# Kernel optimization log

Measured on AMD Instinct MI355X. Metric: run time of the kernel, lower is better.

The kernel has to match this reference:

```python
import jax, jax.numpy as jnp
import numpy as np

S = 8192      # s: number of persons/nodes
F = 1024      # feature_len
A = 256       # attn_len
SIGMA_X, SIGMA_Y = 4.0, 1.0
EPS_VALID = 1e-8
EPS_DIS = 1e-4


def setup_inputs() -> dict:
    key = jax.random.key(0)
    ks = jax.random.split(key, 8)
    batch_data = jax.random.normal(ks[0], (S, F), dtype=jnp.float32)
    xywh = jax.random.uniform(ks[1], (S, 4), dtype=jnp.float32)  # positive -> all rows valid
    actor_weights = jax.random.uniform(ks[2], (S,), dtype=jnp.float32)
    avg_pos = jax.random.uniform(ks[3], (S, 2), dtype=jnp.float32)
    # learned params (kaiming-ish init, zero bias as in original)
    W_h = jax.random.normal(ks[4], (F, 2), dtype=jnp.float32) * (2.0 / F) ** 0.5
    b_h = jnp.zeros((2,), dtype=jnp.float32)
    W_g = jax.random.normal(ks[5], (F, A), dtype=jnp.float32) * (2.0 / F) ** 0.5
    b_g = jnp.zeros((A,), dtype=jnp.float32)
    return {
        "batch_data": batch_data, "xywh": xywh, "OW": 1920, "OH": 1080,
        "actor_weights": actor_weights, "avg_pos": avg_pos,
        "W_h": W_h, "b_h": b_h, "W_g": W_g, "b_g": b_g, "num_person": S,
    }


def reference(batch_data, xywh, OW, OH, actor_weights, avg_pos, W_h, b_h, W_g, b_g, num_person):
    # highlight_fc + tanh -> predicted offsets [S,2]
    hp = jnp.tanh(batch_data @ W_h + b_h)
    hx = hp[:, 0] * xywh[:, 2] * SIGMA_X + xywh[:, 0]  # [S]
    hy = hp[:, 1] * xywh[:, 3] * SIGMA_Y + xywh[:, 1]  # [S]

    # gcn_fc + relu -> node messages [S,A]
    targets = jax.nn.relu(batch_data @ W_g + b_g)

    # valid rows/cols: torch loop skips i/j with sum(xywh) < 1e-8
    valid = jnp.sum(xywh, axis=1) >= EPS_VALID  # [S] bool

    # pairwise inverse-distance weights [S,S] (the memory-bound core)
    dx = hx[:, None] - xywh[None, :, 0]
    dy = hy[:, None] - xywh[None, :, 1]
    dis = jnp.sqrt(dx * dx + dy * dy)
    pair_valid = valid[:, None] & valid[None, :]
    w = jnp.where(pair_valid, 1.0 / (dis + EPS_DIS), 0.0)
    row_sum = jnp.sum(w, axis=1, keepdims=True)
    w = jnp.where(valid[:, None], w / jnp.maximum(row_sum, 1e-30), 0.0)

    targets_weighted = w @ targets  # [S,A]
    return (targets_weighted, hp)
```

## Files before the change

### kernel.cpp

```cpp
#include <hip/hip_runtime.h>
#include <math.h>
#include <stdint.h>

typedef __attribute__((ext_vector_type(8))) short short8;
typedef __attribute__((ext_vector_type(4))) float f32x4;

__device__ __forceinline__ uint32_t cvt_pk_bf16(float lo, float hi) {
  uint32_t r;
  asm("v_cvt_pk_bf16_f32 %0, %1, %2" : "=v"(r) : "v"(lo), "v"(hi));
  return r;
}

__device__ __forceinline__ float wfun(float hx, float hy, float cx, float cy) {
  float dx = hx - cx, dy = hy - cy;
  float d = __builtin_amdgcn_sqrtf(fmaf(dx, dx, dy * dy));
  return __builtin_amdgcn_rcpf(d + 1e-4f);
}

__global__ __launch_bounds__(256) void k_head(
    const float* __restrict__ batch, const float* __restrict__ xywh,
    const float* __restrict__ W_h, const float* __restrict__ b_h,
    float* __restrict__ hp_out, float* __restrict__ hx, float* __restrict__ hy,
    float* __restrict__ validf, float2* __restrict__ cxy, int S, int F) {
  int wid = threadIdx.x >> 6;
  int lane = threadIdx.x & 63;
  int row = blockIdx.x * 4 + wid;
  if (row >= S) return;
  const float4* brow = (const float4*)(batch + (size_t)row * F);
  const float4* wh4 = (const float4*)W_h;
  int nf4 = F >> 2;
  float acc0 = 0.f, acc1 = 0.f;
  for (int k4 = lane; k4 < nf4; k4 += 64) {
    float4 b = brow[k4];
    float4 wa = wh4[2 * k4];
    float4 wb = wh4[2 * k4 + 1];
    acc0 += b.x * wa.x + b.y * wa.z + b.z * wb.x + b.w * wb.z;
    acc1 += b.x * wa.y + b.y * wa.w + b.z * wb.y + b.w * wb.w;
  }
  #pragma unroll
  for (int off = 32; off; off >>= 1) {
    acc0 += __shfl_xor(acc0, off, 64);
    acc1 += __shfl_xor(acc1, off, 64);
  }
  if (lane == 0) {
    float hp0 = tanhf(acc0 + b_h[0]);
    float hp1 = tanhf(acc1 + b_h[1]);
    float4 xy = ((const float4*)xywh)[row];
    hp_out[2 * row] = hp0;
    hp_out[2 * row + 1] = hp1;
    hx[row] = hp0 * xy.z * 4.0f + xy.x;
    hy[row] = hp1 * xy.w * 1.0f + xy.y;
    bool v = (xy.x + xy.y + xy.z + xy.w >= 1e-8f);
    validf[row] = v ? 1.0f : 0.0f;
    cxy[row] = v ? make_float2(xy.x, xy.y) : make_float2(1e30f, 1e30f);
  }
}

__global__ __launch_bounds__(256) void k_prep_w(
    const float* __restrict__ Wg, uint16_t* __restrict__ WgT, int F, int A) {
  int idx = blockIdx.x * 256 + threadIdx.x;
  int a = idx % A;
  int k0 = (idx / A) * 8;
  if (k0 >= F) return;
  float f[8];
  #pragma unroll
  for (int e = 0; e < 8; ++e) f[e] = Wg[(size_t)(k0 + e) * A + a];
  uint4 v;
  v.x = cvt_pk_bf16(f[0], f[1]);
  v.y = cvt_pk_bf16(f[2], f[3]);
  v.z = cvt_pk_bf16(f[4], f[5]);
  v.w = cvt_pk_bf16(f[6], f[7]);
  *(uint4*)(WgT + (size_t)a * F + k0) = v;
}

__global__ __launch_bounds__(256) void k_targets_mfma(
    const float* __restrict__ batch, const uint16_t* __restrict__ WgT,
    const float* __restrict__ bg, uint16_t* __restrict__ tgt2,
    int S, int F, int A) {
  int t = threadIdx.x;
  int lane = t & 63, wid = t >> 6;
  int wm = wid >> 1, wn = wid & 1;
  int i0 = blockIdx.y * 32;
  int row = i0 + wm * 16 + (lane & 15);
  int kch = lane >> 4;
  const float* ab = batch + (size_t)row * F + kch * 8;
  int ncol0 = blockIdx.x * 128 + wn * 64 + (lane & 15);
  const uint16_t* bb = WgT + (size_t)ncol0 * F + kch * 8;

  f32x4 acc[4] = {};
  float4 a0 = *(const float4*)(ab);
  float4 a1 = *(const float4*)(ab + 4);
  short8 bf[4];
  #pragma unroll
  for (int nf = 0; nf < 4; ++nf)
    bf[nf] = *(const short8*)(bb + (size_t)nf * 16 * F);

  for (int k0 = 0; k0 < F; k0 += 32) {
    int kn = (k0 + 32 < F) ? k0 + 32 : 0;
    float4 na0 = *(const float4*)(ab + kn);
    float4 na1 = *(const float4*)(ab + kn + 4);
    short8 nbf[4];
    #pragma unroll
    for (int nf = 0; nf < 4; ++nf)
      nbf[nf] = *(const short8*)(bb + kn + (size_t)nf * 16 * F);
    union { short8 s; uint32_t u[4]; } af;
    af.u[0] = cvt_pk_bf16(a0.x, a0.y);
    af.u[1] = cvt_pk_bf16(a0.z, a0.w);
    af.u[2] = cvt_pk_bf16(a1.x, a1.y);
    af.u[3] = cvt_pk_bf16(a1.z, a1.w);
    #pragma unroll
    for (int nf = 0; nf < 4; ++nf)
      acc[nf] = __builtin_amdgcn_mfma_f32_16x16x32_bf16(af.s, bf[nf], acc[nf], 0, 0, 0);
    a0 = na0; a1 = na1;
    #pragma unroll
    for (int nf = 0; nf < 4; ++nf) bf[nf] = nbf[nf];
  }

  int jb = blockIdx.y;
  int rloc = wm * 16 + (lane >> 4) * 4;
  #pragma unroll
  for (int nf = 0; nf < 4; ++nf) {
    int col = ncol0 + nf * 16;
    float b = bg[col];
    float o0 = fmaxf(acc[nf][0] + b, 0.f);
    float o1 = fmaxf(acc[nf][1] + b, 0.f);
    float o2 = fmaxf(acc[nf][2] + b, 0.f);
    float o3 = fmaxf(acc[nf][3] + b, 0.f);
    uint2 pk;
    pk.x = cvt_pk_bf16(o0, o1);
    pk.y = cvt_pk_bf16(o2, o3);
    *(uint2*)(tgt2 + ((size_t)jb * A + col) * 32 + rloc) = pk;
  }
}

__global__ __launch_bounds__(1024, 4) void k_gather_v17(
    const uint16_t* __restrict__ tgt2, const float2* __restrict__ cxy,
    const float* __restrict__ hx, const float* __restrict__ hy,
    const float* __restrict__ validf, float* __restrict__ out, int S, int A) {
  __shared__ uint16_t Bt[4][256][40];
  __shared__ uint32_t Af[4][2][64][4];
  __shared__ float comb[32][260];
  __shared__ float rs_l[4][32][8];
  __shared__ float scale_s[32];

  int t = threadIdx.x;
  int lane = t & 63, wid = t >> 6;
  int kg = wid >> 2;
  int wn = wid & 3;
  int i0 = blockIdx.x * 32;
  int kch = lane >> 4;
  int n0 = wn * 64 + (lane & 15);
  int NT = S / (4 * 32);
  const size_t TSTRIDE = (size_t)A * 32;

  int wkg = t >> 8;
  int v = t & 255;
  int wr = v & 31;
  int wjp8 = v >> 5;
  float hx_w = hx[i0 + wr], hy_w = hy[i0 + wr];
  int rgw = wr >> 4;
  int L0 = (wr & 15) | ((wjp8 >> 2) << 4);
  int L1 = (wr & 15) | (((wjp8 >> 2) + 2) << 4);
  int sl = wjp8 & 3;
  const float2* gCp = cxy + (size_t)wkg * (S >> 2) + 2 * wjp8;

  int scol = v;
  const uint16_t* gB0 = tgt2 + (size_t)(wkg * NT) * TSTRIDE + (size_t)scol * 32;

  f32x4 acc0[4] = {};
  f32x4 acc1[4] = {};
  float rs = 0.f;

  {
    uint4 q0 = *(const uint4*)(gB0);
    uint4 q1 = *(const uint4*)(gB0 + 8);
    uint4 q2 = *(const uint4*)(gB0 + 16);
    uint4 q3 = *(const uint4*)(gB0 + 24);
    *(uint4*)&Bt[wkg][scol][0]  = q0;
    *(uint4*)&Bt[wkg][scol][8]  = q1;
    *(uint4*)&Bt[wkg][scol][16] = q2;
    *(uint4*)&Bt[wkg][scol][24] = q3;
    float4 ca = *(const float4*)(gCp);
    float4 cb = *(const float4*)(gCp + 16);
    float wA = wfun(hx_w, hy_w, ca.x, ca.y);
    float wB = wfun(hx_w, hy_w, ca.z, ca.w);
    float wC = wfun(hx_w, hy_w, cb.x, cb.y);
    float wD = wfun(hx_w, hy_w, cb.z, cb.w);
    rs += (wA + wB) + (wC + wD);
    Af[wkg][rgw][L0][sl] = cvt_pk_bf16(wA, wB);
    Af[wkg][rgw][L1][sl] = cvt_pk_bf16(wC, wD);
  }
  __syncthreads();
  float4 ccur0 = *(const float4*)(gCp + 32);
  float4 ccur1 = *(const float4*)(gCp + 48);

  for (int ts = 0; ts < NT; ++ts) {
    int tn = (ts + 1 < NT) ? ts + 1 : 0;
    int tf = (ts + 2 < NT) ? ts + 2 : 0;

    const uint16_t* bp = gB0 + (size_t)tn * TSTRIDE;
    uint4 q0 = *(const uint4*)(bp);
    uint4 q1 = *(const uint4*)(bp + 8);
    uint4 q2 = *(const uint4*)(bp + 16);
    uint4 q3 = *(const uint4*)(bp + 24);
    float4 cf0 = *(const float4*)(gCp + (size_t)tf * 32);
    float4 cf1 = *(const float4*)(gCp + (size_t)tf * 32 + 16);

    short8 a0 = *(const short8*)&Af[kg][0][lane][0];
    short8 a1 = *(const short8*)&Af[kg][1][lane][0];
    const uint16_t* br = &Bt[kg][n0][kch * 8];
    short8 b0 = *(const short8*)(br);
    short8 b1 = *(const short8*)(br + 16 * 40);
    short8 b2 = *(const short8*)(br + 32 * 40);
    short8 b3 = *(const short8*)(br + 48 * 40);

    acc0[0] = __builtin_amdgcn_mfma_f32_16x16x32_bf16(a0, b0, acc0[0], 0, 0, 0);
    acc0[1] = __builtin_amdgcn_mfma_f32_16x16x32_bf16(a0, b1, acc0[1], 0, 0, 0);
    acc0[2] = __builtin_amdgcn_mfma_f32_16x16x32_bf16(a0, b2, acc0[2], 0, 0, 0);
    acc0[3] = __builtin_amdgcn_mfma_f32_16x16x32_bf16(a0, b3, acc0[3], 0, 0, 0);
    acc1[0] = __builtin_amdgcn_mfma_f32_16x16x32_bf16(a1, b0, acc1[0], 0, 0, 0);
    acc1[1] = __builtin_amdgcn_mfma_f32_16x16x32_bf16(a1, b1, acc1[1], 0, 0, 0);
    acc1[2] = __builtin_amdgcn_mfma_f32_16x16x32_bf16(a1, b2, acc1[2], 0, 0, 0);
    acc1[3] = __builtin_amdgcn_mfma_f32_16x16x32_bf16(a1, b3, acc1[3], 0, 0, 0);

    float wA = wfun(hx_w, hy_w, ccur0.x, ccur0.y);
    float wB = wfun(hx_w, hy_w, ccur0.z, ccur0.w);
    float wC = wfun(hx_w, hy_w, ccur1.x, ccur1.y);
    float wD = wfun(hx_w, hy_w, ccur1.z, ccur1.w);
    float g = (ts + 1 < NT) ? 1.f : 0.f;
    rs = fmaf(g, (wA + wB) + (wC + wD), rs);
    uint32_t pkA = cvt_pk_bf16(wA, wB);
    uint32_t pkB = cvt_pk_bf16(wC, wD);

    __syncthreads();

    *(uint4*)&Bt[wkg][scol][0]  = q0;
    *(uint4*)&Bt[wkg][scol][8]  = q1;
    *(uint4*)&Bt[wkg][scol][16] = q2;
    *(uint4*)&Bt[wkg][scol][24] = q3;
    Af[wkg][rgw][L0][sl] = pkA;
    Af[wkg][rgw][L1][sl] = pkB;

    __syncthreads();
    ccur0 = cf0;
    ccur1 = cf1;
  }

  rs_l[wkg][wr][wjp8] = rs;
  __syncthreads();
  if (t < 32) {
    float r = 0.f;
    #pragma unroll
    for (int k = 0; k < 4; ++k)
      #pragma unroll
      for (int jp = 0; jp < 8; ++jp) r += rs_l[k][t][jp];
    float fv = validf[i0 + t];
    scale_s[t] = (fv > 0.f) ? 1.0f / fmaxf(r, 1e-30f) : 0.f;
  }
  __syncthreads();

  int rbase = (lane >> 4) * 4;
  #pragma unroll
  for (int round = 1; round < 4; ++round) {
    if (kg == round) {
      #pragma unroll
      for (int r = 0; r < 4; ++r) {
        comb[rbase + r][n0]      = acc0[0][r];
        comb[rbase + r][n0 + 16] = acc0[1][r];
        comb[rbase + r][n0 + 32] = acc0[2][r];
        comb[rbase + r][n0 + 48] = acc0[3][r];
        comb[16 + rbase + r][n0]      = acc1[0][r];
        comb[16 + rbase + r][n0 + 16] = acc1[1][r];
        comb[16 + rbase + r][n0 + 32] = acc1[2][r];
        comb[16 + rbase + r][n0 + 48] = acc1[3][r];
      }
    }
    __syncthreads();
    if (kg == 0) {
      #pragma unroll
      for (int r = 0; r < 4; ++r) {
        acc0[0][r] += comb[rbase + r][n0];
        acc0[1][r] += comb[rbase + r][n0 + 16];
        acc0[2][r] += comb[rbase + r][n0 + 32];
        acc0[3][r] += comb[rbase + r][n0 + 48];
        acc1[0][r] += comb[16 + rbase + r][n0];
        acc1[1][r] += comb[16 + rbase + r][n0 + 16];
        acc1[2][r] += comb[16 + rbase + r][n0 + 32];
        acc1[3][r] += comb[16 + rbase + r][n0 + 48];
      }
    }
    __syncthreads();
  }

  if (kg == 0) {
    #pragma unroll
    for (int r = 0; r < 4; ++r) {
      int row0 = rbase + r;
      float s0 = scale_s[row0];
      size_t base0 = (size_t)(i0 + row0) * A;
      out[base0 + n0]      = acc0[0][r] * s0;
      out[base0 + n0 + 16] = acc0[1][r] * s0;
      out[base0 + n0 + 32] = acc0[2][r] * s0;
      out[base0 + n0 + 48] = acc0[3][r] * s0;
      int row1 = 16 + rbase + r;
      float s1 = scale_s[row1];
      size_t base1 = (size_t)(i0 + row1) * A;
      out[base1 + n0]      = acc1[0][r] * s1;
      out[base1 + n0 + 16] = acc1[1][r] * s1;
      out[base1 + n0 + 32] = acc1[2][r] * s1;
      out[base1 + n0 + 48] = acc1[3][r] * s1;
    }
  }
}

extern "C" void kernel_launch(void* const* d_in, const int* in_sizes, int n_in,
                              void* d_out, int out_size, void* d_ws, size_t ws_size,
                              hipStream_t stream) {
  const float* batch = (const float*)d_in[0];
  const float* xywh  = (const float*)d_in[1];
  const float* W_h   = (const float*)d_in[6];
  const float* b_h   = (const float*)d_in[7];
  const float* W_g   = (const float*)d_in[8];
  const float* b_g   = (const float*)d_in[9];
  int S = in_sizes[4];
  int F = in_sizes[0] / S;
  int A = in_sizes[9];

  float* out    = (float*)d_out;
  float* out_tw = out;
  float* out_hp = out + (size_t)S * A;

  uint16_t* tgt2 = (uint16_t*)d_ws;
  uint16_t* WgT  = tgt2 + (size_t)A * S;
  float* hxv = (float*)(WgT + (size_t)A * F);
  float* hyv = hxv + S;
  float* vfv = hyv + S;
  float2* cxyv = (float2*)(vfv + S);

  k_head<<<dim3((S + 3) / 4), 256, 0, stream>>>(batch, xywh, W_h, b_h,
                                                out_hp, hxv, hyv, vfv, cxyv, S, F);
  k_prep_w<<<dim3((A * F / 8 + 255) / 256), 256, 0, stream>>>(W_g, WgT, F, A);
  k_targets_mfma<<<dim3(A / 128, S / 32), 256, 0, stream>>>(batch, WgT, b_g,
                                                            tgt2, S, F, A);
  k_gather_v17<<<dim3(S / 32), 1024, 0, stream>>>(tgt2, cxyv, hxv, hyv, vfv,
                                                  out_tw, S, A);
}
```

Before: 155.9 us.

## Double-buffer gather LDS with two k-groups and widen targets GEMM tile

The gather kernel drops from four k-split wave groups (1024 threads) to two (512 threads). It double-buffers the Bt/Af shared tiles so only one barrier per iteration is needed, and replaces the three-round cross-group reduction with a single combine step. The targets GEMM now has each block compute all 256 output columns (8 MFMA tiles per wave), so each A row is loaded and converted once instead of twice. The cost is less k-parallelism per block, longer serial loops, and higher register pressure in the GEMM.

```diff
diff --git a/kernel.cpp b/kernel.cpp
--- a/kernel.cpp
+++ b/kernel.cpp
@@ -80,28 +80,28 @@
   int t = threadIdx.x;
   int lane = t & 63, wid = t >> 6;
   int wm = wid >> 1, wn = wid & 1;
-  int i0 = blockIdx.y * 32;
+  int i0 = blockIdx.x * 32;
   int row = i0 + wm * 16 + (lane & 15);
   int kch = lane >> 4;
   const float* ab = batch + (size_t)row * F + kch * 8;
-  int ncol0 = blockIdx.x * 128 + wn * 64 + (lane & 15);
+  int ncol0 = wn * 128 + (lane & 15);
   const uint16_t* bb = WgT + (size_t)ncol0 * F + kch * 8;
 
-  f32x4 acc[4] = {};
+  f32x4 acc[8] = {};
   float4 a0 = *(const float4*)(ab);
   float4 a1 = *(const float4*)(ab + 4);
-  short8 bf[4];
+  short8 bf[8];
   #pragma unroll
-  for (int nf = 0; nf < 4; ++nf)
+  for (int nf = 0; nf < 8; ++nf)
     bf[nf] = *(const short8*)(bb + (size_t)nf * 16 * F);
 
   for (int k0 = 0; k0 < F; k0 += 32) {
     int kn = (k0 + 32 < F) ? k0 + 32 : 0;
     float4 na0 = *(const float4*)(ab + kn);
     float4 na1 = *(const float4*)(ab + kn + 4);
-    short8 nbf[4];
-    #pragma unroll
-    for (int nf = 0; nf < 4; ++nf)
+    short8 nbf[8];
+    #pragma unroll
+    for (int nf = 0; nf < 8; ++nf)
       nbf[nf] = *(const short8*)(bb + kn + (size_t)nf * 16 * F);
     union { short8 s; uint32_t u[4]; } af;
     af.u[0] = cvt_pk_bf16(a0.x, a0.y);
@@ -109,17 +109,17 @@
     af.u[2] = cvt_pk_bf16(a1.x, a1.y);
     af.u[3] = cvt_pk_bf16(a1.z, a1.w);
     #pragma unroll
-    for (int nf = 0; nf < 4; ++nf)
+    for (int nf = 0; nf < 8; ++nf)
       acc[nf] = __builtin_amdgcn_mfma_f32_16x16x32_bf16(af.s, bf[nf], acc[nf], 0, 0, 0);
     a0 = na0; a1 = na1;
     #pragma unroll
-    for (int nf = 0; nf < 4; ++nf) bf[nf] = nbf[nf];
-  }
-
-  int jb = blockIdx.y;
+    for (int nf = 0; nf < 8; ++nf) bf[nf] = nbf[nf];
+  }
+
+  int jb = blockIdx.x;
   int rloc = wm * 16 + (lane >> 4) * 4;
   #pragma unroll
-  for (int nf = 0; nf < 4; ++nf) {
+  for (int nf = 0; nf < 8; ++nf) {
     int col = ncol0 + nf * 16;
     float b = bg[col];
     float o0 = fmaxf(acc[nf][0] + b, 0.f);
@@ -133,14 +133,14 @@
   }
 }
 
-__global__ __launch_bounds__(1024, 4) void k_gather_v17(
+__global__ __launch_bounds__(512, 2) void k_gather_v19(
     const uint16_t* __restrict__ tgt2, const float2* __restrict__ cxy,
     const float* __restrict__ hx, const float* __restrict__ hy,
     const float* __restrict__ validf, float* __restrict__ out, int S, int A) {
-  __shared__ uint16_t Bt[4][256][40];
-  __shared__ uint32_t Af[4][2][64][4];
+  __shared__ uint16_t Bt[2][2][256][40];
+  __shared__ uint32_t Af[2][2][2][64][4];
   __shared__ float comb[32][260];
-  __shared__ float rs_l[4][32][8];
+  __shared__ float rs_l[2][32][8];
   __shared__ float scale_s[32];
 
   int t = threadIdx.x;
@@ -150,8 +150,9 @@
   int i0 = blockIdx.x * 32;
   int kch = lane >> 4;
   int n0 = wn * 64 + (lane & 15);
-  int NT = S / (4 * 32);
+  int NT = (S >> 1) / 32;
   const size_t TSTRIDE = (size_t)A * 32;
+  const int COLS = 40;
 
   int wkg = t >> 8;
   int v = t & 255;
@@ -162,7 +163,11 @@
   int L0 = (wr & 15) | ((wjp8 >> 2) << 4);
   int L1 = (wr & 15) | (((wjp8 >> 2) + 2) << 4);
   int sl = wjp8 & 3;
-  const float2* gCp = cxy + (size_t)wkg * (S >> 2) + 2 * wjp8;
+  uint32_t* af00 = &Af[0][wkg][rgw][L0][sl];
+  uint32_t* af01 = &Af[0][wkg][rgw][L1][sl];
+  uint32_t* af10 = &Af[1][wkg][rgw][L0][sl];
+  uint32_t* af11 = &Af[1][wkg][rgw][L1][sl];
+  const float2* gCp = cxy + (size_t)wkg * (S >> 1) + 2 * wjp8;
 
   int scol = v;
   const uint16_t* gB0 = tgt2 + (size_t)(wkg * NT) * TSTRIDE + (size_t)scol * 32;
@@ -176,10 +181,10 @@
     uint4 q1 = *(const uint4*)(gB0 + 8);
     uint4 q2 = *(const uint4*)(gB0 + 16);
     uint4 q3 = *(const uint4*)(gB0 + 24);
-    *(uint4*)&Bt[wkg][scol][0]  = q0;
-    *(uint4*)&Bt[wkg][scol][8]  = q1;
-    *(uint4*)&Bt[wkg][scol][16] = q2;
-    *(uint4*)&Bt[wkg][scol][24] = q3;
+    *(uint4*)&Bt[0][wkg][scol][0]  = q0;
+    *(uint4*)&Bt[0][wkg][scol][8]  = q1;
+    *(uint4*)&Bt[0][wkg][scol][16] = q2;
+    *(uint4*)&Bt[0][wkg][scol][24] = q3;
     float4 ca = *(const float4*)(gCp);
     float4 cb = *(const float4*)(gCp + 16);
     float wA = wfun(hx_w, hy_w, ca.x, ca.y);
@@ -187,14 +192,15 @@
     float wC = wfun(hx_w, hy_w, cb.x, cb.y);
     float wD = wfun(hx_w, hy_w, cb.z, cb.w);
     rs += (wA + wB) + (wC + wD);
-    Af[wkg][rgw][L0][sl] = cvt_pk_bf16(wA, wB);
-    Af[wkg][rgw][L1][sl] = cvt_pk_bf16(wC, wD);
-  }
-  __syncthreads();
+    *af00 = cvt_pk_bf16(wA, wB);
+    *af01 = cvt_pk_bf16(wC, wD);
+  }
   float4 ccur0 = *(const float4*)(gCp + 32);
   float4 ccur1 = *(const float4*)(gCp + 48);
+  __syncthreads();
 
   for (int ts = 0; ts < NT; ++ts) {
+    int cur = ts & 1, nxt = cur ^ 1;
     int tn = (ts + 1 < NT) ? ts + 1 : 0;
     int tf = (ts + 2 < NT) ? ts + 2 : 0;
 
@@ -206,13 +212,13 @@
     float4 cf0 = *(const float4*)(gCp + (size_t)tf * 32);
     float4 cf1 = *(const float4*)(gCp + (size_t)tf * 32 + 16);
 
-    short8 a0 = *(const short8*)&Af[kg][0][lane][0];
-    short8 a1 = *(const short8*)&Af[kg][1][lane][0];
-    const uint16_t* br = &Bt[kg][n0][kch * 8];
+    short8 a0 = *(const short8*)&Af[cur][kg][0][lane][0];
+    short8 a1 = *(const short8*)&Af[cur][kg][1][lane][0];
+    const uint16_t* br = &Bt[cur][kg][n0][kch * 8];
     short8 b0 = *(const short8*)(br);
-    short8 b1 = *(const short8*)(br + 16 * 40);
-    short8 b2 = *(const short8*)(br + 32 * 40);
-    short8 b3 = *(const short8*)(br + 48 * 40);
+    short8 b1 = *(const short8*)(br + 16 * COLS);
+    short8 b2 = *(const short8*)(br + 32 * COLS);
+    short8 b3 = *(const short8*)(br + 48 * COLS);
 
     acc0[0] = __builtin_amdgcn_mfma_f32_16x16x32_bf16(a0, b0, acc0[0], 0, 0, 0);
     acc0[1] = __builtin_amdgcn_mfma_f32_16x16x32_bf16(a0, b1, acc0[1], 0, 0, 0);
@@ -231,84 +237,61 @@
     rs = fmaf(g, (wA + wB) + (wC + wD), rs);
     uint32_t pkA = cvt_pk_bf16(wA, wB);
     uint32_t pkB = cvt_pk_bf16(wC, wD);
-
-    __syncthreads();
-
-    *(uint4*)&Bt[wkg][scol][0]  = q0;
-    *(uint4*)&Bt[wkg][scol][8]  = q1;
-    *(uint4*)&Bt[wkg][scol][16] = q2;
-    *(uint4*)&Bt[wkg][scol][24] = q3;
-    Af[wkg][rgw][L0][sl] = pkA;
-    Af[wkg][rgw][L1][sl] = pkB;
-
-    __syncthreads();
+    *(nxt ? af10 : af00) = pkA;
+    *(nxt ? af11 : af01) = pkB;
+
+    *(uint4*)&Bt[nxt][wkg][scol][0]  = q0;
+    *(uint4*)&Bt[nxt][wkg][scol][8]  = q1;
+    *(uint4*)&Bt[nxt][wkg][scol][16] = q2;
+    *(uint4*)&Bt[nxt][wkg][scol][24] = q3;
+
     ccur0 = cf0;
     ccur1 = cf1;
+    __syncthreads();
   }
 
   rs_l[wkg][wr][wjp8] = rs;
+
+  int rbase = (lane >> 4) * 4;
+  if (kg == 1) {
+    #pragma unroll
+    for (int r = 0; r < 4; ++r) {
+      comb[rbase + r][n0]      = acc0[0][r];
+      comb[rbase + r][n0 + 16] = acc0[1][r];
+      comb[rbase + r][n0 + 32] = acc0[2][r];
+      comb[rbase + r][n0 + 48] = acc0[3][r];
+      comb[16 + rbase + r][n0]      = acc1[0][r];
+      comb[16 + rbase + r][n0 + 16] = acc1[1][r];
+      comb[16 + rbase + r][n0 + 32] = acc1[2][r];
+      comb[16 + rbase + r][n0 + 48] = acc1[3][r];
+    }
+  }
   __syncthreads();
   if (t < 32) {
     float r = 0.f;
     #pragma unroll
-    for (int k = 0; k < 4; ++k)
-      #pragma unroll
-      for (int jp = 0; jp < 8; ++jp) r += rs_l[k][t][jp];
+    for (int jp = 0; jp < 8; ++jp) r += rs_l[0][t][jp] + rs_l[1][t][jp];
     float fv = validf[i0 + t];
     scale_s[t] = (fv > 0.f) ? 1.0f / fmaxf(r, 1e-30f) : 0.f;
   }
   __syncthreads();
-
-  int rbase = (lane >> 4) * 4;
-  #pragma unroll
-  for (int round = 1; round < 4; ++round) {
-    if (kg == round) {
-      #pragma unroll
-      for (int r = 0; r < 4; ++r) {
-        comb[rbase + r][n0]      = acc0[0][r];
-        comb[rbase + r][n0 + 16] = acc0[1][r];
-        comb[rbase + r][n0 + 32] = acc0[2][r];
-        comb[rbase + r][n0 + 48] = acc0[3][r];
-        comb[16 + rbase + r][n0]      = acc1[0][r];
-        comb[16 + rbase + r][n0 + 16] = acc1[1][r];
-        comb[16 + rbase + r][n0 + 32] = acc1[2][r];
-        comb[16 + rbase + r][n0 + 48] = acc1[3][r];
-      }
-    }
-    __syncthreads();
-    if (kg == 0) {
-      #pragma unroll
-      for (int r = 0; r < 4; ++r) {
-        acc0[0][r] += comb[rbase + r][n0];
-        acc0[1][r] += comb[rbase + r][n0 + 16];
-        acc0[2][r] += comb[rbase + r][n0 + 32];
-        acc0[3][r] += comb[rbase + r][n0 + 48];
-        acc1[0][r] += comb[16 + rbase + r][n0];
-        acc1[1][r] += comb[16 + rbase + r][n0 + 16];
-        acc1[2][r] += comb[16 + rbase + r][n0 + 32];
-        acc1[3][r] += comb[16 + rbase + r][n0 + 48];
-      }
-    }
-    __syncthreads();
-  }
-
   if (kg == 0) {
     #pragma unroll
     for (int r = 0; r < 4; ++r) {
       int row0 = rbase + r;
       float s0 = scale_s[row0];
       size_t base0 = (size_t)(i0 + row0) * A;
-      out[base0 + n0]      = acc0[0][r] * s0;
-      out[base0 + n0 + 16] = acc0[1][r] * s0;
-      out[base0 + n0 + 32] = acc0[2][r] * s0;
-      out[base0 + n0 + 48] = acc0[3][r] * s0;
+      out[base0 + n0]      = (acc0[0][r] + comb[row0][n0]) * s0;
+      out[base0 + n0 + 16] = (acc0[1][r] + comb[row0][n0 + 16]) * s0;
+      out[base0 + n0 + 32] = (acc0[2][r] + comb[row0][n0 + 32]) * s0;
+      out[base0 + n0 + 48] = (acc0[3][r] + comb[row0][n0 + 48]) * s0;
       int row1 = 16 + rbase + r;
       float s1 = scale_s[row1];
       size_t base1 = (size_t)(i0 + row1) * A;
-      out[base1 + n0]      = acc1[0][r] * s1;
-      out[base1 + n0 + 16] = acc1[1][r] * s1;
-      out[base1 + n0 + 32] = acc1[2][r] * s1;
-      out[base1 + n0 + 48] = acc1[3][r] * s1;
+      out[base1 + n0]      = (acc1[0][r] + comb[row1][n0]) * s1;
+      out[base1 + n0 + 16] = (acc1[1][r] + comb[row1][n0 + 16]) * s1;
+      out[base1 + n0 + 32] = (acc1[2][r] + comb[row1][n0 + 32]) * s1;
+      out[base1 + n0 + 48] = (acc1[3][r] + comb[row1][n0 + 48]) * s1;
     }
   }
 }
@@ -340,8 +323,7 @@
   k_head<<<dim3((S + 3) / 4), 256, 0, stream>>>(batch, xywh, W_h, b_h,
                                                 out_hp, hxv, hyv, vfv, cxyv, S, F);
   k_prep_w<<<dim3((A * F / 8 + 255) / 256), 256, 0, stream>>>(W_g, WgT, F, A);
-  k_targets_mfma<<<dim3(A / 128, S / 32), 256, 0, stream>>>(batch, WgT, b_g,
-                                                            tgt2, S, F, A);
-  k_gather_v17<<<dim3(S / 32), 1024, 0, stream>>>(tgt2, cxyv, hxv, hyv, vfv,
-                                                  out_tw, S, A);
-}
+  k_targets_mfma<<<dim3(S / 32), 256, 0, stream>>>(batch, WgT, b_g, tgt2, S, F, A);
+  k_gather_v19<<<dim3(S / 32), 512, 0, stream>>>(tgt2, cxyv, hxv, hyv, vfv,
+                                                 out_tw, S, A);
+}
```

Result: slower. 160.9 us (+3.2%).
